# Optimization experiments

Measured on AMD Instinct MI355X. Metric: run time of the kernel, lower is better.

Reference implementation:

```python
import jax, jax.numpy as jnp
import numpy as np

B, C, HW_IMG = 8, 64, 128
BLOCK_W, STRIDE, KERNEL = 16, 2, 3


def _pam(x, Wq, bq, Wk, bk, Wv, bv):
    # Position attention module on a window x: [B, C, h, w]
    b, c, h, w = x.shape
    xf = x.reshape(b, c, h * w)                         # [B, C, N]
    q = jnp.einsum('dc,bcn->bdn', Wq, xf) + bq[None, :, None]
    k = jnp.einsum('dc,bcn->bdn', Wk, xf) + bk[None, :, None]
    v = jnp.einsum('dc,bcn->bdn', Wv, xf) + bv[None, :, None]
    # energy[b,i,j] = sum_c q[b,c,i] * k[b,c,j]; softmax over j
    attn = jax.nn.softmax(jnp.einsum('bci,bcj->bij', q, k), axis=-1)  # [B, N, N]
    out = jnp.einsum('bcj,bij->bci', v, attn)           # [B, C, N]
    return out.reshape(b, c, h, w) + x


def _block_sa(x, params):
    # Overlapping-window self-attention; later windows overwrite earlier ones,
    # each window reads from the ORIGINAL x (matching the torch clone semantics).
    out = x
    nmax = int(HW_IMG / (BLOCK_W * STRIDE))  # = 4
    for i in range(nmax + 1):
        sx = i * BLOCK_W * STRIDE
        if sx >= HW_IMG:
            continue
        ex = min(sx + BLOCK_W * KERNEL, HW_IMG)
        for j in range(nmax + 1):
            sy = j * BLOCK_W * STRIDE
            if sy >= HW_IMG:
                continue
            ey = min(sy + BLOCK_W * KERNEL, HW_IMG)
            win = _pam(x[:, :, sx:ex, sy:ey], *params)
            out = out.at[:, :, sx:ex, sy:ey].set(win)
    return out


def setup_inputs() -> dict:
    key = jax.random.key(0)
    ks = jax.random.split(key, 13)
    x = jax.random.normal(ks[0], (B, C, HW_IMG, HW_IMG), dtype=jnp.float32)
    s = 1.0 / np.sqrt(C)
    d = {'x': x}
    names = ['Wq1', 'Wk1', 'Wv1', 'Wq2', 'Wk2', 'Wv2']
    for n, k in zip(names, ks[1:7]):
        d[n] = jax.random.normal(k, (C, C), dtype=jnp.float32) * s
    bnames = ['bq1', 'bk1', 'bv1', 'bq2', 'bk2', 'bv2']
    for n, k in zip(bnames, ks[7:13]):
        d[n] = jax.random.normal(k, (C,), dtype=jnp.float32) * 0.01
    return d


def reference(x, Wq1, Wk1, Wv1, Wq2, Wk2, Wv2, bq1, bk1, bv1, bq2, bk2, bv2):
    x = _block_sa(x, (Wq1, bq1, Wk1, bk1, Wv1, bv1))
    x = _block_sa(x, (Wq2, bq2, Wk2, bk2, Wv2, bv2))
    return x
```

## Files before the change

### kernel.cpp

```cpp
#include <hip/hip_runtime.h>
#include <hip/hip_bf16.h>

typedef __attribute__((ext_vector_type(8))) __bf16 bf16x8;
typedef __attribute__((ext_vector_type(4))) __bf16 bf16x4;
typedef __attribute__((ext_vector_type(8))) _Float16 f16x8;
typedef __attribute__((ext_vector_type(4))) _Float16 f16x4;
typedef __attribute__((ext_vector_type(4))) float f32x4;

#define LOG2E 1.44269504088896340736f

__device__ inline f32x4 mfma16(bf16x8 a, bf16x8 b, f32x4 c) {
  return __builtin_amdgcn_mfma_f32_16x16x32_bf16(a, b, c, 0, 0, 0);
}
__device__ inline f32x4 mfma16h(f16x8 a, f16x8 b, f32x4 c) {
  return __builtin_amdgcn_mfma_f32_16x16x32_f16(a, b, c, 0, 0, 0);
}

__device__ inline int rowdiv(int kg, int w) {
  return (w == 32) ? (kg >> 5) : ((kg * 43691) >> 21);
}

__global__ __launch_bounds__(256) void proj_kernel(
    const float* __restrict__ X, const float* __restrict__ Wq,
    const float* __restrict__ Wk, const float* __restrict__ Wv,
    const float* __restrict__ bq, const float* __restrict__ bv,
    _Float16* __restrict__ QT, _Float16* __restrict__ KT,
    _Float16* __restrict__ Vc)
{
  const int b = blockIdx.y;
  const int pixbase = blockIdx.x * 256;
  const int t = threadIdx.x;
  __shared__ __align__(16) __bf16 xs[256 * 128];

  {
    const float* xp = X + (size_t)b * 64 * 16384 + pixbase + t;
    #pragma unroll
    for (int c8 = 0; c8 < 8; ++c8) {
      bf16x8 vh, vl;
      #pragma unroll
      for (int i = 0; i < 8; ++i) {
        float x = xp[(size_t)(c8 * 8 + i) * 16384];
        __bf16 h = (__bf16)x;
        vh[i] = h;
        vl[i] = (__bf16)(x - (float)h);
      }
      int col = (c8 * 8) ^ ((t & 7) << 3);
      *(bf16x8*)&xs[t * 128 + col] = vh;
      *(bf16x8*)&xs[t * 128 + 64 + col] = vl;
    }
  }
  __syncthreads();

  const int wv = t >> 6, lane = t & 63, g = lane >> 4, lq = lane & 15;

  bf16x8 xf[4][2][2];
  #pragma unroll
  for (int nt = 0; nt < 4; ++nt)
    #pragma unroll
    for (int ks = 0; ks < 2; ++ks) {
      int pixl = wv * 64 + nt * 16 + lq;
      int col = (ks * 32 + g * 8) ^ ((pixl & 7) << 3);
      xf[nt][ks][0] = *(bf16x8*)&xs[pixl * 128 + col];
      xf[nt][ks][1] = *(bf16x8*)&xs[pixl * 128 + 64 + col];
    }

  #pragma unroll
  for (int mat = 0; mat < 3; ++mat) {
    const float* Wm = (mat == 0) ? Wq : (mat == 1) ? Wk : Wv;
    #pragma unroll
    for (int mt = 0; mt < 4; ++mt) {
      bf16x8 wh[2], wl[2];
      #pragma unroll
      for (int ks = 0; ks < 2; ++ks) {
        const float* wp = Wm + (mt * 16 + lq) * 64 + ks * 32 + g * 8;
        f32x4 w0 = *(const f32x4*)wp;
        f32x4 w1 = *(const f32x4*)(wp + 4);
        bf16x8 fh, fl;
        #pragma unroll
        for (int r = 0; r < 4; ++r) {
          __bf16 h0 = (__bf16)w0[r]; fh[r] = h0; fl[r] = (__bf16)(w0[r] - (float)h0);
          __bf16 h1 = (__bf16)w1[r]; fh[4 + r] = h1; fl[4 + r] = (__bf16)(w1[r] - (float)h1);
        }
        wh[ks] = fh; wl[ks] = fl;
      }
      f32x4 binit = {0.f, 0.f, 0.f, 0.f};
      if (mat == 0) binit = *(const f32x4*)(bq + mt * 16 + g * 4);
      if (mat == 2) binit = *(const f32x4*)(bv + mt * 16 + g * 4);
      f32x4 acc[4];
      #pragma unroll
      for (int nt = 0; nt < 4; ++nt) acc[nt] = binit;
      #pragma unroll
      for (int nt = 0; nt < 4; ++nt)
        #pragma unroll
        for (int ks = 0; ks < 2; ++ks) {
          acc[nt] = mfma16(wh[ks], xf[nt][ks][0], acc[nt]);
          acc[nt] = mfma16(wh[ks], xf[nt][ks][1], acc[nt]);
          acc[nt] = mfma16(wl[ks], xf[nt][ks][0], acc[nt]);
        }
      #pragma unroll
      for (int nt = 0; nt < 4; ++nt) {
        int pix = pixbase + wv * 64 + nt * 16 + lq;
        if (mat == 2) {
          #pragma unroll
          for (int r = 0; r < 4; ++r)
            Vc[((size_t)b * 64 + mt * 16 + g * 4 + r) * 16384 + pix] = (_Float16)acc[nt][r];
        } else if (mat == 0) {
          f16x4 oh, ol;
          #pragma unroll
          for (int r = 0; r < 4; ++r) {
            float v = acc[nt][r] * LOG2E;
            _Float16 h = (_Float16)v;
            oh[r] = h;
            ol[r] = (_Float16)(v - (float)h);
          }
          _Float16* dst = QT + ((size_t)b * 16384 + pix) * 128 + mt * 16 + g * 4;
          *(f16x4*)dst = oh;
          *(f16x4*)(dst + 64) = ol;
        } else {
          f16x4 oh;
          #pragma unroll
          for (int r = 0; r < 4; ++r) oh[r] = (_Float16)acc[nt][r];
          *(f16x4*)(KT + ((size_t)b * 16384 + pix) * 64 + mt * 16 + g * 4) = oh;
        }
      }
    }
  }
}

__global__ __launch_bounds__(256, 2) void attn_kernel(
    const _Float16* __restrict__ QT, const _Float16* __restrict__ KT,
    const _Float16* __restrict__ Vc, const float* RES, float* OUT)
{
  const int i = blockIdx.x;
  const int b = i & 7;
  const int s_lin = i >> 3;
  const int wo = s_lin >> 2;
  const int qb = s_lin & 3;
  int win;
  {
    int w3 = (wo * 11) >> 5;
    win = (wo < 9) ? (wo + w3) : ((wo < 12) ? (3 + ((wo - 9) << 2)) : wo);
  }
  const int wi = win >> 2, wj = win & 3;
  const int sx = wi * 32, sy = wj * 32;
  const int w = (128 - sy) < 48 ? (128 - sy) : 48;
  const int h = (128 - sx) < 48 ? (128 - sx) : 48;
  const int Nk = h * w, nch = Nk >> 6;
  const int t = threadIdx.x;
  const int wv = t >> 6, lane = t & 63, g = lane >> 4, lq = lane & 15;

  __shared__ __align__(16) _Float16 lp[4][64 * 64];

  const int r0 = sx + qb * 8 + wv * 2;
  f16x8 qf[4][2][2];
  #pragma unroll
  for (int qt = 0; qt < 4; ++qt) {
    int qpix = (r0 + (qt >> 1)) * 128 + sy + (qt & 1) * 16 + lq;
    const _Float16* qp = QT + ((size_t)b * 16384 + qpix) * 128;
    qf[qt][0][0] = *(const f16x8*)(qp + g * 8);
    qf[qt][1][0] = *(const f16x8*)(qp + 32 + g * 8);
    qf[qt][0][1] = *(const f16x8*)(qp + 64 + g * 8);
    qf[qt][1][1] = *(const f16x8*)(qp + 96 + g * 8);
  }

  f32x4 O[4][4];
  #pragma unroll
  for (int qt = 0; qt < 4; ++qt)
    #pragma unroll
    for (int cht = 0; cht < 4; ++cht) O[qt][cht] = (f32x4){0.f, 0.f, 0.f, 0.f};
  float m[4] = {-__builtin_inff(), -__builtin_inff(), -__builtin_inff(), -__builtin_inff()};
  float l[4] = {0.f, 0.f, 0.f, 0.f};

  for (int ch = 0; ch < nch; ++ch) {
    const int kbase = ch * 64;

    f32x4 s[4][4];
    #pragma unroll
    for (int qt = 0; qt < 4; ++qt)
      #pragma unroll
      for (int t4 = 0; t4 < 4; ++t4) s[qt][t4] = (f32x4){0.f, 0.f, 0.f, 0.f};
    #pragma unroll
    for (int t4 = 0; t4 < 4; ++t4) {
      int kg = kbase + t4 * 16 + lq;
      int kr = rowdiv(kg, w), kc = kg - kr * w;
      const _Float16* kp = KT + ((size_t)b * 16384 + (sx + kr) * 128 + sy + kc) * 64 + g * 8;
      f16x8 kh0 = *(const f16x8*)(kp);
      f16x8 kh1 = *(const f16x8*)(kp + 32);
      __builtin_amdgcn_s_setprio(1);
      #pragma unroll
      for (int qt = 0; qt < 4; ++qt) {
        s[qt][t4] = mfma16h(kh0, qf[qt][0][0], s[qt][t4]);
        s[qt][t4] = mfma16h(kh0, qf[qt][0][1], s[qt][t4]);
        s[qt][t4] = mfma16h(kh1, qf[qt][1][0], s[qt][t4]);
        s[qt][t4] = mfma16h(kh1, qf[qt][1][1], s[qt][t4]);
      }
      __builtin_amdgcn_s_setprio(0);
    }

    #pragma unroll
    for (int qt = 0; qt < 4; ++qt) {
      float cm = -__builtin_inff();
      #pragma unroll
      for (int t4 = 0; t4 < 4; ++t4)
        #pragma unroll
        for (int r = 0; r < 4; ++r) cm = fmaxf(cm, s[qt][t4][r]);
      cm = fmaxf(cm, __shfl_xor(cm, 16));
      cm = fmaxf(cm, __shfl_xor(cm, 32));
      if (__any(cm > m[qt] + 8.0f)) {
        float mnew = fmaxf(m[qt], cm);
        float sc = exp2f(m[qt] - mnew);
        m[qt] = mnew;
        l[qt] *= sc;
        #pragma unroll
        for (int cht = 0; cht < 4; ++cht) O[qt][cht] *= sc;
      }
      float ps = 0.f;
      int rowb = (qt * 16 + lq) * 64;
      #pragma unroll
      for (int t4 = 0; t4 < 4; ++t4) {
        float p0 = exp2f(s[qt][t4][0] - m[qt]);
        float p1 = exp2f(s[qt][t4][1] - m[qt]);
        float p2 = exp2f(s[qt][t4][2] - m[qt]);
        float p3 = exp2f(s[qt][t4][3] - m[qt]);
        ps += (p0 + p1) + (p2 + p3);
        f16x4 ph;
        ph[0] = (_Float16)p0;
        ph[1] = (_Float16)p1;
        ph[2] = (_Float16)p2;
        ph[3] = (_Float16)p3;
        int col = (t4 * 16 + g * 4) ^ ((lq & 7) << 3);
        *(f16x4*)&lp[wv][rowb + col] = ph;
      }
      ps += __shfl_xor(ps, 16);
      ps += __shfl_xor(ps, 32);
      l[qt] += ps;
    }

    #pragma unroll
    for (int ks = 0; ks < 2; ++ks) {
      int kg = kbase + ks * 32 + g * 8;
      int kr = rowdiv(kg, w), kc = kg - kr * w;
      size_t vpo = (size_t)b * 64 * 16384 + (size_t)((sx + kr) * 128 + sy + kc);
      f16x8 vf[4];
      #pragma unroll
      for (int cht = 0; cht < 4; ++cht)
        vf[cht] = *(const f16x8*)(Vc + vpo + (size_t)(cht * 16 + lq) * 16384);
      int pcol = (ks * 32 + g * 8) ^ ((lq & 7) << 3);
      #pragma unroll
      for (int qt = 0; qt < 4; ++qt) {
        int rowb = (qt * 16 + lq) * 64;
        f16x8 pb = *(f16x8*)&lp[wv][rowb + pcol];
        __builtin_amdgcn_s_setprio(1);
        #pragma unroll
        for (int cht = 0; cht < 4; ++cht)
          O[qt][cht] = mfma16h(vf[cht], pb, O[qt][cht]);
        __builtin_amdgcn_s_setprio(0);
      }
    }
  }

  #pragma unroll
  for (int qt = 0; qt < 4; ++qt) {
    float inv = 1.0f / l[qt];
    int qpix = (r0 + (qt >> 1)) * 128 + sy + (qt & 1) * 16 + lq;
    #pragma unroll
    for (int cht = 0; cht < 4; ++cht)
      #pragma unroll
      for (int r = 0; r < 4; ++r) {
        int chn = cht * 16 + g * 4 + r;
        size_t idx = ((size_t)b * 64 + chn) * 16384 + qpix;
        OUT[idx] = O[qt][cht][r] * inv + RES[idx];
      }
  }
}

extern "C" void kernel_launch(void* const* d_in, const int* in_sizes, int n_in,
                              void* d_out, int out_size, void* d_ws, size_t ws_size,
                              hipStream_t stream) {
  const float* x   = (const float*)d_in[0];
  const float* Wq1 = (const float*)d_in[1];
  const float* Wk1 = (const float*)d_in[2];
  const float* Wv1 = (const float*)d_in[3];
  const float* Wq2 = (const float*)d_in[4];
  const float* Wk2 = (const float*)d_in[5];
  const float* Wv2 = (const float*)d_in[6];
  const float* bq1 = (const float*)d_in[7];
  const float* bv1 = (const float*)d_in[9];
  const float* bq2 = (const float*)d_in[10];
  const float* bv2 = (const float*)d_in[12];
  float* out = (float*)d_out;

  const size_t IMG = (size_t)8 * 16384;
  _Float16* QT = (_Float16*)d_ws;
  _Float16* KT = QT + IMG * 128;
  _Float16* Vc = KT + IMG * 64;

  dim3 pgrid(64, 8);
  proj_kernel<<<pgrid, 256, 0, stream>>>(x, Wq1, Wk1, Wv1, bq1, bv1, QT, KT, Vc);
  attn_kernel<<<512, 256, 0, stream>>>(QT, KT, Vc, x, out);
  proj_kernel<<<pgrid, 256, 0, stream>>>(out, Wq2, Wk2, Wv2, bq2, bv2, QT, KT, Vc);
  attn_kernel<<<512, 256, 0, stream>>>(QT, KT, Vc, out, out);
}
```

Baseline: 463.5 us.

## Stage K/V chunks into double-buffered LDS via async global_load_lds

Each 64-key chunk of K and V is now copied cooperatively into swizzled, double-buffered shared memory with direct global-to-LDS DMA, and the next chunk is prefetched while the current one is computed. The four waves previously each loaded the same K/V data straight from global memory, so this removes redundant global traffic and hides load latency. In exchange it adds 32KB of LDS per block, which may lower occupancy, plus a block-wide barrier per chunk. The sync placement relies on the async DMA having finished by the barrier.

```diff
diff --git a/kernel.cpp b/kernel.cpp
--- a/kernel.cpp
+++ b/kernel.cpp
@@ -18,6 +18,12 @@
 
 __device__ inline int rowdiv(int kg, int w) {
   return (w == 32) ? (kg >> 5) : ((kg * 43691) >> 21);
+}
+
+__device__ __forceinline__ void dma16(const void* g, void* l) {
+  __builtin_amdgcn_global_load_lds(
+      (const __attribute__((address_space(1))) void*)g,
+      (__attribute__((address_space(3))) void*)l, 16, 0, 0);
 }
 
 __global__ __launch_bounds__(256) void proj_kernel(
@@ -149,6 +155,8 @@
   const int t = threadIdx.x;
   const int wv = t >> 6, lane = t & 63, g = lane >> 4, lq = lane & 15;
 
+  __shared__ __align__(16) _Float16 kbuf[2][64 * 64];
+  __shared__ __align__(16) _Float16 vbuf[2][64 * 64];
   __shared__ __align__(16) _Float16 lp[4][64 * 64];
 
   const int r0 = sx + qb * 8 + wv * 2;
@@ -171,8 +179,36 @@
   float m[4] = {-__builtin_inff(), -__builtin_inff(), -__builtin_inff(), -__builtin_inff()};
   float l[4] = {0.f, 0.f, 0.f, 0.f};
 
+  auto stage = [&](int bu, int kbase) {
+    #pragma unroll
+    for (int j = 0; j < 2; ++j) {
+      int s = j * 256 + t;
+      int key = s >> 3, u = s & 7;
+      int su = u ^ (key & 7);
+      int kg = kbase + key;
+      int kr = rowdiv(kg, w), kc = kg - kr * w;
+      const _Float16* gp = KT + ((size_t)b * 16384 + (sx + kr) * 128 + sy + kc) * 64 + su * 8;
+      dma16(gp, &kbuf[bu][(size_t)(j * 256 + wv * 64) * 8]);
+    }
+    #pragma unroll
+    for (int j = 0; j < 2; ++j) {
+      int s = j * 256 + t;
+      int chn = s >> 3, u = s & 7;
+      int su = u ^ (chn & 7);
+      int kg0 = kbase + su * 8;
+      int kr = rowdiv(kg0, w);
+      int pix = (sx + kr) * 128 + sy + kg0 - kr * w;
+      const _Float16* gp = Vc + ((size_t)b * 64 + chn) * 16384 + pix;
+      dma16(gp, &vbuf[bu][(size_t)(j * 256 + wv * 64) * 8]);
+    }
+  };
+
+  stage(0, 0);
+  __syncthreads();
+
   for (int ch = 0; ch < nch; ++ch) {
-    const int kbase = ch * 64;
+    const int cur = ch & 1;
+    if (ch + 1 < nch) stage(cur ^ 1, (ch + 1) * 64);
 
     f32x4 s[4][4];
     #pragma unroll
@@ -181,11 +217,11 @@
       for (int t4 = 0; t4 < 4; ++t4) s[qt][t4] = (f32x4){0.f, 0.f, 0.f, 0.f};
     #pragma unroll
     for (int t4 = 0; t4 < 4; ++t4) {
-      int kg = kbase + t4 * 16 + lq;
-      int kr = rowdiv(kg, w), kc = kg - kr * w;
-      const _Float16* kp = KT + ((size_t)b * 16384 + (sx + kr) * 128 + sy + kc) * 64 + g * 8;
-      f16x8 kh0 = *(const f16x8*)(kp);
-      f16x8 kh1 = *(const f16x8*)(kp + 32);
+      int row = t4 * 16 + lq;
+      const _Float16* kp = &kbuf[cur][row * 64];
+      int sw = row & 7;
+      f16x8 kh0 = *(const f16x8*)&kp[(g ^ sw) * 8];
+      f16x8 kh1 = *(const f16x8*)&kp[((g + 4) ^ sw) * 8];
       __builtin_amdgcn_s_setprio(1);
       #pragma unroll
       for (int qt = 0; qt < 4; ++qt) {
@@ -238,13 +274,12 @@
 
     #pragma unroll
     for (int ks = 0; ks < 2; ++ks) {
-      int kg = kbase + ks * 32 + g * 8;
-      int kr = rowdiv(kg, w), kc = kg - kr * w;
-      size_t vpo = (size_t)b * 64 * 16384 + (size_t)((sx + kr) * 128 + sy + kc);
       f16x8 vf[4];
       #pragma unroll
-      for (int cht = 0; cht < 4; ++cht)
-        vf[cht] = *(const f16x8*)(Vc + vpo + (size_t)(cht * 16 + lq) * 16384);
+      for (int cht = 0; cht < 4; ++cht) {
+        int chrow = cht * 16 + lq;
+        vf[cht] = *(const f16x8*)&vbuf[cur][chrow * 64 + (((ks * 4 + g) ^ (chrow & 7)) * 8)];
+      }
       int pcol = (ks * 32 + g * 8) ^ ((lq & 7) << 3);
       #pragma unroll
       for (int qt = 0; qt < 4; ++qt) {
@@ -257,6 +292,8 @@
         __builtin_amdgcn_s_setprio(0);
       }
     }
+
+    __syncthreads();
   }
 
   #pragma unroll
```

After: 405.5 us. -12.5%, faster.
